# Optimization experiments

Hardware: AMD Instinct MI355X
Metric: run time of the kernel (lower is better)

Reference implementation:

```python
import jax, jax.numpy as jnp
import numpy as np


def setup_inputs() -> dict:
    key = jax.random.key(0)
    k1, k2, k3, k4 = jax.random.split(key, 4)
    B, I, P, F = 4096, 1024, 512, 2048
    x = jax.random.normal(k1, (B, I), dtype=jnp.float32)
    # params initialized like torch.rand(...)*2-1 (uniform in [-1,1])
    features = jax.random.uniform(k2, (F, I), dtype=jnp.float32, minval=-1.0, maxval=1.0)
    prototypes = jax.random.uniform(k3, (P, I), dtype=jnp.float32, minval=-1.0, maxval=1.0)
    # scalars: torch inits to zeros; use small nonzero values so output/grads are informative
    abt = jax.random.normal(k4, (3,), dtype=jnp.float32) * 0.1
    alpha = abt[0:1]
    beta = abt[1:2]
    theta = abt[2:3]
    return {"x": x, "features": features, "prototypes": prototypes,
            "alpha": alpha, "beta": beta, "theta": theta}


def reference(x, features, prototypes, alpha, beta, theta):
    # x: [b, i], features: [f, i], prototypes: [p, i]
    # Original einsums broadcast over p but the projection is p-independent:
    xf = x @ features.T            # [b, f]
    pf = prototypes @ features.T   # [p, f]
    x_pres = jax.nn.relu(xf)       # [b, f]
    p_pres = jax.nn.relu(pf)       # [p, f]
    # common[b,p]       = sum_f xf*pf*relu(xf)*relu(pf)
    # x_distinct[b,p]   = sum_f xf*relu(xf)*(1-relu(pf))
    # p_distinct[b,p]   = sum_f pf*relu(pf)*(1-relu(xf))
    a = xf * x_pres                # [b, f]
    c = pf * p_pres                # [p, f]
    common = a @ c.T                                   # [b, p]
    x_distinctive = a @ (1.0 - p_pres).T               # [b, p]
    p_distinctive = (1.0 - x_pres) @ c.T               # [b, p]
    return theta * common - alpha * x_distinctive - beta * p_distinctive
```

## Files before the change

kernel.cpp:

```cpp
#include <hip/hip_runtime.h>
#include <cstdint>

typedef __attribute__((ext_vector_type(8))) short bf16x8;
typedef __attribute__((ext_vector_type(4))) float f32x4;
typedef __attribute__((ext_vector_type(4))) float f4;
typedef __attribute__((ext_vector_type(4))) unsigned short u16x4;
typedef unsigned short u16;

__device__ __forceinline__ u16 f2bf(float f) {
  uint32_t u = __builtin_bit_cast(uint32_t, f);
  u += 0x7fffu + ((u >> 16) & 1u);
  return (u16)(u >> 16);
}

__device__ __forceinline__ void async_cp16(const void* g, void* l) {
  __builtin_amdgcn_global_load_lds(
      (const __attribute__((address_space(1))) uint32_t*)g,
      (__attribute__((address_space(3))) uint32_t*)l, 16, 0, 0);
}

__global__ __launch_bounds__(256) void cast3(
    const float* __restrict__ x, const float* __restrict__ f,
    const float* __restrict__ p, u16* __restrict__ dst,
    int n1, int n2, int n3) {
  int i = (blockIdx.x * 256 + threadIdx.x) * 4;
  const float* src;
  int local;
  if (i < n1) { src = x; local = i; }
  else if (i < n1 + n2) { src = f; local = i - n1; }
  else if (i < n1 + n2 + n3) { src = p; local = i - n1 - n2; }
  else return;
  f4 v = *(const f4*)(src + local);
  u16x4 o;
  o.x = f2bf(v.x); o.y = f2bf(v.y); o.z = f2bf(v.z); o.w = f2bf(v.w);
  *(u16x4*)(dst + i) = o;
}

__global__ __launch_bounds__(256) void zero_f32(float* __restrict__ p, int n4) {
  int i = blockIdx.x * 256 + threadIdx.x;
  if (i < n4) ((f4*)p)[i] = (f4){0.f, 0.f, 0.f, 0.f};
}

template<int TM, int TN>
__device__ __forceinline__ void mainloop(
    const u16* __restrict__ A, const u16* __restrict__ B, int K,
    int kbeg, int kend, int tid, u16* lds, f32x4 (&acc)[TM / 32][TN / 32]) {
  constexpr int BK = 64;
  constexpr int WM = TM / 2, WN = TN / 2;
  constexpr int MT = TM / 32, NT = TN / 32;
  const int lane = tid & 63;
  const int wave = tid >> 6;
  const int wrow = wave >> 1, wcol = wave & 1;

  for (int k0 = kbeg; k0 < kend; k0 += BK) {
    #pragma unroll
    for (int it = 0; it < TM / 32; ++it) {
      int c = it * 256 + tid;
      int row = c >> 3, pc = c & 7;
      int gc = pc ^ (row & 7);
      async_cp16(A + (size_t)row * K + (k0 + gc * 8),
                 &lds[(it * 256 + wave * 64) * 8]);
    }
    #pragma unroll
    for (int it = 0; it < TN / 32; ++it) {
      int c = it * 256 + tid;
      int row = c >> 3, pc = c & 7;
      int gc = pc ^ (row & 7);
      async_cp16(B + (size_t)row * K + (k0 + gc * 8),
                 &lds[TM * BK + (it * 256 + wave * 64) * 8]);
    }
    __syncthreads();

    #pragma unroll
    for (int s = 0; s < 2; ++s) {
      const int h = s * 4 + (lane >> 4);
      bf16x8 afr[MT], bfr[NT];
      #pragma unroll
      for (int i = 0; i < MT; ++i) {
        int r = wrow * WM + i * 16 + (lane & 15);
        afr[i] = *(const bf16x8*)&lds[(r * 8 + (h ^ (r & 7))) * 8];
      }
      #pragma unroll
      for (int j = 0; j < NT; ++j) {
        int r = wcol * WN + j * 16 + (lane & 15);
        bfr[j] = *(const bf16x8*)&lds[TM * BK + (r * 8 + (h ^ (r & 7))) * 8];
      }
      #pragma unroll
      for (int i = 0; i < MT; ++i)
        #pragma unroll
        for (int j = 0; j < NT; ++j)
          acc[i][j] = __builtin_amdgcn_mfma_f32_16x16x32_bf16(afr[i], bfr[j], acc[i][j], 0, 0, 0);
    }
    __syncthreads();
  }
}

__global__ __launch_bounds__(256) void gemm12(
    const u16* __restrict__ xb, const u16* __restrict__ pb,
    const u16* __restrict__ fb, u16* __restrict__ Acat, u16* __restrict__ Bcat,
    const float* __restrict__ alpha, const float* __restrict__ beta,
    const float* __restrict__ theta) {
  constexpr int TM = 128, TN = 64, K = 1024, N = 2048;
  constexpr int WM = TM / 2, WN = TN / 2;
  constexpr int MT = TM / 32, NT = TN / 32;
  __shared__ u16 lds[(TM + TN) * 64];

  const int tid = threadIdx.x;
  const int lane = tid & 63;
  const int wave = tid >> 6;
  const int wrow = wave >> 1, wcol = wave & 1;
  const int bm_all = blockIdx.x * TM;
  const int bn = blockIdx.y * TN;
  const bool is_x = bm_all < 4096;
  const u16* A = is_x ? xb + (size_t)bm_all * K : pb + (size_t)(bm_all - 4096) * K;
  const u16* B = fb + (size_t)bn * K;

  f32x4 acc[MT][NT] = {};
  mainloop<TM, TN>(A, B, K, 0, K, tid, lds, acc);

  float th = 0.f, al = 0.f, be = 0.f;
  if (!is_x) { th = theta[0]; al = alpha[0]; be = beta[0]; }
  u16* dst = is_x ? Acat : Bcat;
  const int rbase = is_x ? bm_all : bm_all - 4096;

  #pragma unroll
  for (int i = 0; i < MT; ++i) {
    const int gr0 = rbase + wrow * WM + i * 16 + (lane >> 4) * 4;
    #pragma unroll
    for (int j = 0; j < NT; ++j) {
      const int gc = bn + wcol * WN + j * 16 + (lane & 15);
      #pragma unroll
      for (int r = 0; r < 4; ++r) {
        float v = acc[i][j][r];
        float pres = v > 0.f ? v : 0.f;
        float o1, o2;
        if (is_x) { o1 = v * pres; o2 = 1.f - pres; }
        else { float cc = v * pres; o1 = th * cc - al * (1.f - pres); o2 = -be * cc; }
        size_t base = (size_t)(gr0 + r) * (size_t)(2 * N) + gc;
        dst[base]     = f2bf(o1);
        dst[base + N] = f2bf(o2);
      }
    }
  }
}

__global__ __launch_bounds__(256) void gemm3(
    const u16* __restrict__ Acat, const u16* __restrict__ Bcat,
    float* __restrict__ out) {
  constexpr int TM = 128, TN = 64, K = 4096, N = 512, KSPLIT = 4;
  constexpr int WM = TM / 2, WN = TN / 2;
  constexpr int MT = TM / 32, NT = TN / 32;
  __shared__ u16 lds[(TM + TN) * 64];

  const int tid = threadIdx.x;
  const int lane = tid & 63;
  const int wave = tid >> 6;
  const int wrow = wave >> 1, wcol = wave & 1;
  const int bm = blockIdx.x * TM;
  const int bn = blockIdx.y * TN;
  const int kbeg = blockIdx.z * (K / KSPLIT);
  const int kend = kbeg + (K / KSPLIT);

  f32x4 acc[MT][NT] = {};
  mainloop<TM, TN>(Acat + (size_t)bm * K, Bcat + (size_t)bn * K, K, kbeg, kend,
                   tid, lds, acc);

  #pragma unroll
  for (int i = 0; i < MT; ++i) {
    const int gr0 = bm + wrow * WM + i * 16 + (lane >> 4) * 4;
    #pragma unroll
    for (int j = 0; j < NT; ++j) {
      const int gc = bn + wcol * WN + j * 16 + (lane & 15);
      #pragma unroll
      for (int r = 0; r < 4; ++r)
        unsafeAtomicAdd(&out[(size_t)(gr0 + r) * N + gc], acc[i][j][r]);
    }
  }
}

extern "C" void kernel_launch(void* const* d_in, const int* in_sizes, int n_in,
                              void* d_out, int out_size, void* d_ws, size_t ws_size,
                              hipStream_t stream) {
  const float* x     = (const float*)d_in[0];
  const float* feat  = (const float*)d_in[1];
  const float* proto = (const float*)d_in[2];
  const float* alpha = (const float*)d_in[3];
  const float* beta  = (const float*)d_in[4];
  const float* theta = (const float*)d_in[5];
  float* out = (float*)d_out;

  constexpr int Bb = 4096, Ii = 1024, Pp = 512, Ff = 2048;

  char* ws = (char*)d_ws;
  size_t off = 0;
  u16* xb   = (u16*)(ws + off); off += (size_t)Bb * Ii * 2;
  u16* fb   = (u16*)(ws + off); off += (size_t)Ff * Ii * 2;
  u16* pb   = (u16*)(ws + off); off += (size_t)Pp * Ii * 2;
  u16* Acat = (u16*)(ws + off); off += (size_t)Bb * 2 * Ff * 2;
  u16* Bcat = (u16*)(ws + off);

  const int n1 = Bb * Ii, n2 = Ff * Ii, n3 = Pp * Ii;
  cast3<<<((n1 + n2 + n3) / 4 + 255) / 256, 256, 0, stream>>>(
      x, feat, proto, xb, n1, n2, n3);

  zero_f32<<<(Bb * Pp / 4 + 255) / 256, 256, 0, stream>>>(out, Bb * Pp / 4);

  gemm12<<<dim3(36, 32), 256, 0, stream>>>(xb, pb, fb, Acat, Bcat, alpha, beta, theta);

  gemm3<<<dim3(Bb / 128, Pp / 64, 4), 256, 0, stream>>>(Acat, Bcat, out);
}
```

Baseline: 165.0 us.

## Enlarge GEMM tiles, stage epilogue through LDS, replace atomics with partial-sum reduction

```diff
diff --git a/kernel.cpp b/kernel.cpp
--- a/kernel.cpp
+++ b/kernel.cpp
@@ -5,6 +5,7 @@
 typedef __attribute__((ext_vector_type(4))) float f32x4;
 typedef __attribute__((ext_vector_type(4))) float f4;
 typedef __attribute__((ext_vector_type(4))) unsigned short u16x4;
+typedef __attribute__((ext_vector_type(8))) unsigned short u16x8;
 typedef unsigned short u16;
 
 __device__ __forceinline__ u16 f2bf(float f) {
@@ -36,11 +37,6 @@
   *(u16x4*)(dst + i) = o;
 }
 
-__global__ __launch_bounds__(256) void zero_f32(float* __restrict__ p, int n4) {
-  int i = blockIdx.x * 256 + threadIdx.x;
-  if (i < n4) ((f4*)p)[i] = (f4){0.f, 0.f, 0.f, 0.f};
-}
-
 template<int TM, int TN>
 __device__ __forceinline__ void mainloop(
     const u16* __restrict__ A, const u16* __restrict__ B, int K,
@@ -100,10 +96,10 @@
     const u16* __restrict__ fb, u16* __restrict__ Acat, u16* __restrict__ Bcat,
     const float* __restrict__ alpha, const float* __restrict__ beta,
     const float* __restrict__ theta) {
-  constexpr int TM = 128, TN = 64, K = 1024, N = 2048;
-  constexpr int WM = TM / 2, WN = TN / 2;
+  constexpr int TM = 128, TN = 128, K = 1024, N = 2048;
   constexpr int MT = TM / 32, NT = TN / 32;
-  __shared__ u16 lds[(TM + TN) * 64];
+  constexpr int TSTRIDE = 136;
+  __shared__ u16 lds[TM * TSTRIDE];
 
   const int tid = threadIdx.x;
   const int lane = tid & 63;
@@ -121,60 +117,92 @@
   float th = 0.f, al = 0.f, be = 0.f;
   if (!is_x) { th = theta[0]; al = alpha[0]; be = beta[0]; }
   u16* dst = is_x ? Acat : Bcat;
-  const int rbase = is_x ? bm_all : bm_all - 4096;
+  const int rowbase = is_x ? bm_all : bm_all - 4096;
 
   #pragma unroll
-  for (int i = 0; i < MT; ++i) {
-    const int gr0 = rbase + wrow * WM + i * 16 + (lane >> 4) * 4;
-    #pragma unroll
-    for (int j = 0; j < NT; ++j) {
-      const int gc = bn + wcol * WN + j * 16 + (lane & 15);
-      #pragma unroll
-      for (int r = 0; r < 4; ++r) {
-        float v = acc[i][j][r];
-        float pres = v > 0.f ? v : 0.f;
-        float o1, o2;
-        if (is_x) { o1 = v * pres; o2 = 1.f - pres; }
-        else { float cc = v * pres; o1 = th * cc - al * (1.f - pres); o2 = -be * cc; }
-        size_t base = (size_t)(gr0 + r) * (size_t)(2 * N) + gc;
-        dst[base]     = f2bf(o1);
-        dst[base + N] = f2bf(o2);
+  for (int half = 0; half < 2; ++half) {
+    __syncthreads();
+    #pragma unroll
+    for (int i = 0; i < MT; ++i) {
+      #pragma unroll
+      for (int j = 0; j < NT; ++j) {
+        const int cl = wcol * 64 + j * 16 + (lane & 15);
+        #pragma unroll
+        for (int r = 0; r < 4; ++r) {
+          const int rl = wrow * 64 + i * 16 + (lane >> 4) * 4 + r;
+          float v = acc[i][j][r];
+          float pres = v > 0.f ? v : 0.f;
+          float o;
+          if (is_x) o = half == 0 ? v * pres : 1.f - pres;
+          else {
+            float cc = v * pres;
+            o = half == 0 ? th * cc - al * (1.f - pres) : -be * cc;
+          }
+          lds[rl * TSTRIDE + cl] = f2bf(o);
+        }
       }
+    }
+    __syncthreads();
+    #pragma unroll
+    for (int v = 0; v < 8; ++v) {
+      const int rl = v * 16 + (tid >> 4);
+      const int cl = (tid & 15) * 8;
+      u16x8 vec = *(const u16x8*)&lds[rl * TSTRIDE + cl];
+      *(u16x8*)&dst[(size_t)(rowbase + rl) * (2 * N) + bn + cl + half * N] = vec;
     }
   }
 }
 
 __global__ __launch_bounds__(256) void gemm3(
     const u16* __restrict__ Acat, const u16* __restrict__ Bcat,
-    float* __restrict__ out) {
-  constexpr int TM = 128, TN = 64, K = 4096, N = 512, KSPLIT = 4;
-  constexpr int WM = TM / 2, WN = TN / 2;
+    float* __restrict__ part) {
+  constexpr int TM = 128, TN = 128, K = 4096, KSPLIT = 4;
   constexpr int MT = TM / 32, NT = TN / 32;
   __shared__ u16 lds[(TM + TN) * 64];
 
+  const int tid = threadIdx.x;
+  const int bm = blockIdx.x * TM;
+  const int bn = blockIdx.y * TN;
+  const int kbeg = blockIdx.z * (K / KSPLIT);
+  const int kend = kbeg + (K / KSPLIT);
+
+  f32x4 acc[MT][NT] = {};
+  mainloop<TM, TN>(Acat + (size_t)bm * K, Bcat + (size_t)bn * K, K, kbeg, kend,
+                   tid, lds, acc);
+
+  const size_t pbase =
+      ((size_t)blockIdx.z * 128 + blockIdx.y * 32 + blockIdx.x) * 16384;
+  #pragma unroll
+  for (int i = 0; i < MT; ++i)
+    #pragma unroll
+    for (int j = 0; j < NT; ++j)
+      *(f4*)&part[pbase + (i * 4 + j) * 1024 + tid * 4] = acc[i][j];
+}
+
+__global__ __launch_bounds__(256) void reduce4(
+    const float* __restrict__ part, float* __restrict__ out) {
+  constexpr int N = 512;
   const int tid = threadIdx.x;
   const int lane = tid & 63;
   const int wave = tid >> 6;
   const int wrow = wave >> 1, wcol = wave & 1;
-  const int bm = blockIdx.x * TM;
-  const int bn = blockIdx.y * TN;
-  const int kbeg = blockIdx.z * (K / KSPLIT);
-  const int kend = kbeg + (K / KSPLIT);
-
-  f32x4 acc[MT][NT] = {};
-  mainloop<TM, TN>(Acat + (size_t)bm * K, Bcat + (size_t)bn * K, K, kbeg, kend,
-                   tid, lds, acc);
+  const int tileId = blockIdx.x;
+  const int bm = (tileId & 31) * 128;
+  const int bn = (tileId >> 5) * 128;
 
   #pragma unroll
-  for (int i = 0; i < MT; ++i) {
-    const int gr0 = bm + wrow * WM + i * 16 + (lane >> 4) * 4;
-    #pragma unroll
-    for (int j = 0; j < NT; ++j) {
-      const int gc = bn + wcol * WN + j * 16 + (lane & 15);
-      #pragma unroll
-      for (int r = 0; r < 4; ++r)
-        unsafeAtomicAdd(&out[(size_t)(gr0 + r) * N + gc], acc[i][j][r]);
-    }
+  for (int s = 0; s < 16; ++s) {
+    f4 v = {0.f, 0.f, 0.f, 0.f};
+    #pragma unroll
+    for (int z = 0; z < 4; ++z)
+      v += *(const f4*)&part[((size_t)z * 128 + tileId) * 16384 + s * 1024 + tid * 4];
+    const int i = s >> 2, j = s & 3;
+    const int gr0 = bm + wrow * 64 + i * 16 + (lane >> 4) * 4;
+    const int gc = bn + wcol * 64 + j * 16 + (lane & 15);
+    out[(size_t)(gr0 + 0) * N + gc] = v.x;
+    out[(size_t)(gr0 + 1) * N + gc] = v.y;
+    out[(size_t)(gr0 + 2) * N + gc] = v.z;
+    out[(size_t)(gr0 + 3) * N + gc] = v.w;
   }
 }
 
@@ -192,20 +220,21 @@
   constexpr int Bb = 4096, Ii = 1024, Pp = 512, Ff = 2048;
 
   char* ws = (char*)d_ws;
-  size_t off = 0;
-  u16* xb   = (u16*)(ws + off); off += (size_t)Bb * Ii * 2;
-  u16* fb   = (u16*)(ws + off); off += (size_t)Ff * Ii * 2;
-  u16* pb   = (u16*)(ws + off); off += (size_t)Pp * Ii * 2;
-  u16* Acat = (u16*)(ws + off); off += (size_t)Bb * 2 * Ff * 2;
-  u16* Bcat = (u16*)(ws + off);
+  u16* xb    = (u16*)ws;
+  u16* fb    = xb + (size_t)Bb * Ii;
+  u16* pb    = fb + (size_t)Ff * Ii;
+  float* part = (float*)ws;
+  size_t r0 = (size_t)4 * 128 * 16384 * 4;
+  u16* Acat = (u16*)(ws + r0);
+  u16* Bcat = Acat + (size_t)Bb * 2 * Ff;
 
   const int n1 = Bb * Ii, n2 = Ff * Ii, n3 = Pp * Ii;
   cast3<<<((n1 + n2 + n3) / 4 + 255) / 256, 256, 0, stream>>>(
       x, feat, proto, xb, n1, n2, n3);
 
-  zero_f32<<<(Bb * Pp / 4 + 255) / 256, 256, 0, stream>>>(out, Bb * Pp / 4);
-
-  gemm12<<<dim3(36, 32), 256, 0, stream>>>(xb, pb, fb, Acat, Bcat, alpha, beta, theta);
-
-  gemm3<<<dim3(Bb / 128, Pp / 64, 4), 256, 0, stream>>>(Acat, Bcat, out);
-}
+  gemm12<<<dim3(36, 16), 256, 0, stream>>>(xb, pb, fb, Acat, Bcat, alpha, beta, theta);
+
+  gemm3<<<dim3(Bb / 128, Pp / 128, 4), 256, 0, stream>>>(Acat, Bcat, part);
+
+  reduce4<<<128, 256, 0, stream>>>(part, out);
+}
```

Result: faster. 155.0 us (-6.1%).
